# Kernel tuning notes

Measured on AMD Instinct MI355X. Metric: run time of the kernel, lower is better.

## Reference

```python
import jax, jax.numpy as jnp
import numpy as np
from jax import lax

# ---- static config (from BasePllay_2 / AdTopoLayer(out_features=50, T=25, m0=0.2, lims=[[224,0],[0,224]], K_max=2, p=0)) ----
H = W = 28
G = H * W
T = 25
K_MAX = 2
M0 = 0.2
OUT_FEATURES = 50
B = 32
TSEQ = jnp.linspace(0.0, 100.0, T)  # fixed landscape sample grid (covers DTM value range)

# static grid geometry from lims=[[224,0],[0,224]]
_xs = np.linspace(224.0, 0.0, H)
_ys = np.linspace(0.0, 224.0, W)
_pts = np.stack(np.meshgrid(_xs, _ys, indexing="ij"), -1).reshape(G, 2)
_d = np.sqrt(((_pts[:, None] - _pts[None]) ** 2).sum(-1))
_sidx = np.argsort(_d, axis=-1)
SDIST = jnp.asarray(np.take_along_axis(_d, _sidx, -1), jnp.float32)  # [G,G] sorted distances per grid point
SIDX = jnp.asarray(_sidx.astype(np.int32))                            # [G,G] static distance-sort order

# 4-connectivity neighbor table for the cubical (pixel) grid, -1 = invalid
_ii = np.arange(G).reshape(H, W)
_nb = np.full((H, W, 4), -1, np.int32)
_nb[1:, :, 0] = _ii[:-1, :]
_nb[:-1, :, 1] = _ii[1:, :]
_nb[:, 1:, 2] = _ii[:, :-1]
_nb[:, :-1, 3] = _ii[:, 1:]
NBR = jnp.asarray(_nb.reshape(G, 4))


def dtm(w):
    """Weighted distance-to-measure (r=2) on the fixed grid. w: [B,G] nonneg -> [B,G]."""
    sw = w[:, SIDX]                               # [B,G,G] weights in distance order
    cw = jnp.cumsum(sw, -1)
    d2 = SDIST ** 2
    cwd = jnp.cumsum(sw * d2[None], -1)
    bound = M0 * w.sum(-1)                        # [B]
    k = jnp.argmax(cw >= bound[:, None, None], -1)  # [B,G] first index reaching mass bound
    km1 = jnp.maximum(k - 1, 0)
    take = lambda a, i: jnp.take_along_axis(a, i[..., None], -1)[..., 0]
    has_prev = k > 0
    cw_p = jnp.where(has_prev, take(cw, km1), 0.0)
    cwd_p = jnp.where(has_prev, take(cwd, km1), 0.0)
    dk2 = d2[jnp.arange(G)[None, :], k]           # [B,G]
    val = (cwd_p + (bound[:, None] - cw_p) * dk2) / bound[:, None]
    return jnp.sqrt(jnp.maximum(val, 0.0))


def pd0(vals):
    """0-dim sublevel-set persistence of vals on the pixel grid (union-find, elder rule).
    Returns (births[G], deaths[G]); non-merging pixels yield zero-persistence pairs,
    essential components die at the max filtration value."""
    order = jnp.argsort(vals).astype(jnp.int32)
    rank = jnp.zeros(G, jnp.int32).at[order].set(jnp.arange(G, dtype=jnp.int32))

    def find(parent, i):
        return lax.while_loop(lambda j: parent[j] != j, lambda j: parent[j], i)

    def step(s, carry):
        parent, death = carry
        p = order[s]
        best = p
        for t in range(4):  # unrolled over the 4 grid neighbors (static)
            q = NBR[p, t]
            ok = (q >= 0) & (rank[jnp.maximum(q, 0)] < s)  # neighbor already inserted
            r = find(parent, jnp.where(ok, q, p))
            merge = ok & (r != best)
            r_old = rank[r] < rank[best]
            older = jnp.where(r_old, r, best)
            younger = jnp.where(r_old, best, r)
            widx = jnp.where(merge, younger, G)   # slot G is a dummy
            parent = parent.at[widx].set(older)
            death = death.at[widx].set(p)         # younger component dies at pixel p
            best = jnp.where(merge, older, best)
        return parent, death

    parent0 = jnp.arange(G + 1, dtype=jnp.int32)
    death0 = jnp.full(G + 1, -1, jnp.int32)
    _, death = lax.fori_loop(0, G, step, (parent0, death0))
    d = death[:G]
    deaths = jnp.where(d >= 0, vals[jnp.maximum(d, 0)], vals.max())
    return vals, deaths


def landscape(births, deaths):
    """K_MAX persistence landscapes sampled at TSEQ. [B,G] -> [B, K_MAX*T]."""
    tb = TSEQ[None, :, None] - births[:, None, :]   # [B,T,G]
    td = deaths[:, None, :] - TSEQ[None, :, None]
    tent = jnp.maximum(jnp.minimum(tb, td), 0.0)
    topk = lax.top_k(tent, K_MAX)[0]                # [B,T,K]
    return jnp.transpose(topk, (0, 2, 1)).reshape(births.shape[0], K_MAX * T)


def _forward(x, w_land, b_land, w_fc, b_fc):
    w = x.reshape(x.shape[0], -1)          # nn.Flatten: pixel intensities as measure weights
    v = dtm(w)                             # [B,G]
    births, deaths = jax.vmap(pd0)(v)
    feats = landscape(births, deaths)      # [B, 50]
    xt = feats @ w_land.T + b_land         # AdTopoLayer output [B, out_features]
    signal = jnp.abs(lax.stop_gradient(xt)).sum(0)   # torch: x.detach().abs().sum(0)
    out = jnp.maximum(xt, 0.0) @ w_fc.T + b_fc       # fc(relu(x))
    return out, signal

_forward_jit = jax.jit(_forward)


def setup_inputs() -> dict:
    key = jax.random.key(0)
    k = jax.random.split(key, 4)
    x = jax.random.uniform(k[0], (B, 1, H, W), jnp.float32)  # image-like nonneg weights
    w_land = jax.random.normal(k[1], (OUT_FEATURES, K_MAX * T), jnp.float32) * 0.1
    b_land = jnp.zeros((OUT_FEATURES,), jnp.float32)
    w_fc = jax.random.normal(k[2], (10, OUT_FEATURES), jnp.float32) * 0.1
    b_fc = jnp.zeros((10,), jnp.float32)
    return {"x": x, "w_land": w_land, "b_land": b_land, "w_fc": w_fc, "b_fc": b_fc}


def reference(x, w_land, b_land, w_fc, b_fc):
    return _forward_jit(x, w_land, b_land, w_fc, b_fc)
```

## Files before the change

kernel.cpp:

```cpp
#include <hip/hip_runtime.h>
#include <math.h>

#define H28 28
#define G784 784
#define BATCH 32
#define NOFF 3025
#define NOFFP 3072
#define NKEY 1459
#define TPTS 25
#define KMAX 2
#define NFEAT 50
#define OUTF 50
#define NCLS 10

#define NBX 16
#define BT 512
#define BT2 512

struct OffPair { unsigned ij; float d2; };
struct OffTab  { OffPair e[NOFFP]; };

constexpr double csqrt(double x) {
  double r = x * 0.5 + 1.0;
  for (int i = 0; i < 20; i++) r = 0.5 * (r + x / r);
  return r;
}

constexpr OffTab make_offtab() {
  OffTab t{};
  int start[NKEY] = {};
  for (int i = 0; i < NOFF; i++) {
    int di = i / 55 - 27, dj = i % 55 - 27;
    start[di * di + dj * dj]++;
  }
  int run = 0;
  for (int k = 0; k < NKEY; k++) { int h = start[k]; start[k] = run; run += h; }
  for (int i = 0; i < NOFF; i++) {
    int di = i / 55 - 27, dj = i % 55 - 27;
    int key = di * di + dj * dj;
    int pos = start[key]++;
    float sd = (key == 0) ? 0.0f : (float)(csqrt((double)key) * (224.0 / 27.0));
    t.e[pos].ij = ((unsigned)(di & 0xffff)) | (((unsigned)(dj & 0xffff)) << 16);
    t.e[pos].d2 = sd * sd;
  }
  for (int i = NOFF; i < NOFFP; i++) { t.e[i].ij = 0x00640064u; t.e[i].d2 = 0.f; }
  return t;
}

__device__ constexpr OffTab OFFTAB = make_offtab();

__device__ __forceinline__ float wave_iscan_f32(float x) {
  int t;
  t = __builtin_amdgcn_update_dpp(0, __float_as_int(x), 0x111, 0xf, 0xf, true);
  x += __int_as_float(t);
  t = __builtin_amdgcn_update_dpp(0, __float_as_int(x), 0x112, 0xf, 0xf, true);
  x += __int_as_float(t);
  t = __builtin_amdgcn_update_dpp(0, __float_as_int(x), 0x114, 0xf, 0xf, true);
  x += __int_as_float(t);
  t = __builtin_amdgcn_update_dpp(0, __float_as_int(x), 0x118, 0xf, 0xf, true);
  x += __int_as_float(t);
  t = __builtin_amdgcn_update_dpp(0, __float_as_int(x), 0x142, 0xa, 0xf, true);
  x += __int_as_float(t);
  t = __builtin_amdgcn_update_dpp(0, __float_as_int(x), 0x143, 0xc, 0xf, true);
  x += __int_as_float(t);
  return x;
}

__global__ __launch_bounds__(BT) void dtm_kernel(const float* __restrict__ x,
                                                 float* __restrict__ v,
                                                 int* __restrict__ done_ctr) {
  __shared__ float w_s[G784];
  __shared__ float red[BT];

  const int tid = threadIdx.x;
  const int b   = blockIdx.x;
  const int bx  = blockIdx.y;

  if (b == 0 && bx == 0 && tid == 0) *done_ctr = 0;

  float ps = 0.f;
  for (int i = tid; i < G784; i += BT) {
    float wv = x[b * G784 + i];
    w_s[i] = wv;
    ps += wv;
  }
  red[tid] = ps;
  __syncthreads();
  for (int off = BT / 2; off > 0; off >>= 1) {
    if (tid < off) red[tid] += red[tid + off];
    __syncthreads();
  }
  const float bound = 0.2f * red[0];

  const int wave = tid >> 6;
  const int lane = tid & 63;
  const int slot = bx * 8 + wave;

  for (int g = slot; g < G784; g += NBX * 8) {
    const int i1 = g / H28, j1 = g % H28;
    float cw = 0.f, cwd = 0.f;
    float cwp = 0.f, cwdp = 0.f, dk2 = 0.f;
    bool crossed = false;
    int o = lane;
    unsigned ij = OFFTAB.e[o].ij;
    float d2v   = OFFTAB.e[o].d2;
    for (int base = 0; base < NOFFP && !crossed; base += 64) {
      int onext = o + 64;
      if (onext >= NOFFP) onext = o;
      const unsigned ij_n = OFFTAB.e[onext].ij;
      const float    d2_n = OFFTAB.e[onext].d2;
      const int di = (short)(ij & 0xffffu);
      const int dj = (short)(ij >> 16);
      const int i2 = i1 + di, j2 = j1 + dj;
      const bool inb = ((unsigned)i2 < (unsigned)H28) & ((unsigned)j2 < (unsigned)H28);
      const float wv = inb ? w_s[i2 * H28 + j2] : 0.f;
      const float wd = wv * d2v;
      const float psw = wave_iscan_f32(wv);
      const float psd = wave_iscan_f32(wd);
      const unsigned long long mask = __ballot(cw + psw >= bound);
      if (mask) {
        const int f = __ffsll((unsigned long long)mask) - 1;
        const float psw_f = __shfl(psw, f);
        const float w_f   = __shfl(wv, f);
        const float psd_f = __shfl(psd, f);
        const float wd_f  = __shfl(wd, f);
        dk2  = __shfl(d2v, f);
        cwp  = cw + (psw_f - w_f);
        cwdp = cwd + (psd_f - wd_f);
        crossed = true;
      } else {
        cw  += __int_as_float(__builtin_amdgcn_readlane(__float_as_int(psw), 63));
        cwd += __int_as_float(__builtin_amdgcn_readlane(__float_as_int(psd), 63));
      }
      ij = ij_n; d2v = d2_n; o = onext;
    }
    const float val = (cwdp + (bound - cwp) * dk2) / bound;
    if (lane == 0) v[b * G784 + g] = sqrtf(fmaxf(val, 0.f));
  }
}

__device__ __forceinline__ unsigned long long pix_key(const float* val_s, int p) {
  return (((unsigned long long)__float_as_uint(val_s[p])) << 10) | (unsigned)p;
}

__global__ __launch_bounds__(BT2) void pd0_kernel(const float* __restrict__ v,
                                                  float* __restrict__ feats,
                                                  int* __restrict__ done_ctr,
                                                  const float* __restrict__ w_land,
                                                  const float* __restrict__ b_land,
                                                  const float* __restrict__ w_fc,
                                                  const float* __restrict__ b_fc,
                                                  float* __restrict__ out) {
  __shared__ float val_s[G784];
  __shared__ int   ptr_s[G784];
  __shared__ int   parent[G784];
  __shared__ float deathv[G784];
  __shared__ int   mlist[G784];
  __shared__ unsigned long long edges[2048];
  __shared__ float redf[BT2];
  __shared__ int   mcnt_sh, ecnt_sh, last_sh;
  __shared__ float vmax_sh;
  __shared__ float f_s[BATCH * NFEAT];
  __shared__ float xt_s[BATCH * OUTF];

  const int tid = threadIdx.x;
  const int b   = blockIdx.x;
  if (tid == 0) { mcnt_sh = 0; ecnt_sh = 0; }

  float pm = -1e30f;
  for (int i = tid; i < G784; i += BT2) {
    float xv = v[b * G784 + i];
    val_s[i] = xv;
    pm = fmaxf(pm, xv);
  }
  redf[tid] = pm;
  __syncthreads();
  for (int off = BT2 / 2; off > 0; off >>= 1) {
    if (tid < off) redf[tid] = fmaxf(redf[tid], redf[tid + off]);
    __syncthreads();
  }
  if (tid == 0) vmax_sh = redf[0];
  __syncthreads();
  const float vmax = vmax_sh;

  for (int p = tid; p < G784; p += BT2) {
    unsigned long long kp = pix_key(val_s, p);
    int i = p / H28, j = p % H28;
    int nbs[4];
    nbs[0] = (i > 0)       ? p - H28 : -1;
    nbs[1] = (i < H28 - 1) ? p + H28 : -1;
    nbs[2] = (j > 0)       ? p - 1   : -1;
    nbs[3] = (j < H28 - 1) ? p + 1   : -1;
    int best = p;
    unsigned long long bk = kp;
    for (int t = 0; t < 4; t++) {
      int q = nbs[t];
      if (q >= 0) {
        unsigned long long kq = pix_key(val_s, q);
        if (kq < bk) { bk = kq; best = q; }
      }
    }
    ptr_s[p]  = best;
    parent[p] = p;
    deathv[p] = vmax;
    if (best == p) {
      int mi = atomicAdd(&mcnt_sh, 1);
      mlist[mi] = p;
    }
  }
  __syncthreads();

  for (int r = 0; r < 10; r++) {
    for (int p = tid; p < G784; p += BT2) ptr_s[p] = ptr_s[ptr_s[p]];
    __syncthreads();
  }

  for (int p = tid; p < G784; p += BT2) {
    unsigned long long kp = pix_key(val_s, p);
    int i = p / H28, j = p % H28;
    int nbs[4];
    nbs[0] = (i > 0)       ? p - H28 : -1;
    nbs[1] = (i < H28 - 1) ? p + H28 : -1;
    nbs[2] = (j > 0)       ? p - 1   : -1;
    nbs[3] = (j < H28 - 1) ? p + 1   : -1;
    int bp = ptr_s[p];
    for (int t = 0; t < 4; t++) {
      int q = nbs[t];
      if (q >= 0) {
        unsigned long long kq = pix_key(val_s, q);
        int bq = ptr_s[q];
        if (kq < kp && bq != bp) {
          int e = atomicAdd(&ecnt_sh, 1);
          if (e < 2048)
            edges[e] = (((unsigned long long)__float_as_uint(val_s[p])) << 32) |
                       (((unsigned long long)(unsigned)p) << 22) |
                       (((unsigned long long)(unsigned)t) << 20) |
                       (((unsigned long long)(unsigned)bp) << 10) |
                       ((unsigned long long)(unsigned)bq);
        }
      }
    }
  }
  __syncthreads();
  const int ecnt = (ecnt_sh < 2048) ? ecnt_sh : 2048;
  const int mcnt = mcnt_sh;

  int n2 = 2;
  while (n2 < ecnt) n2 <<= 1;
  for (int i = ecnt + tid; i < n2; i += BT2) edges[i] = ~0ULL;
  __syncthreads();
  for (int kk = 2; kk <= n2; kk <<= 1) {
    for (int jj = kk >> 1; jj > 0; jj >>= 1) {
      for (int i = tid; i < n2; i += BT2) {
        int ixj = i ^ jj;
        if (ixj > i) {
          unsigned long long a = edges[i], c = edges[ixj];
          bool up = ((i & kk) == 0);
          if ((a > c) == up) { edges[i] = c; edges[ixj] = a; }
        }
      }
      __syncthreads();
    }
  }

  if (tid < 64) {
    const int target = mcnt - 1;
    int merged = 0;
    for (int base = 0; base < ecnt && merged < target; base += 64) {
      int i = base + tid;
      bool valid = (i < ecnt);
      unsigned long long e = valid ? edges[i] : 0ULL;
      int A = (int)((e >> 10) & 1023u);
      int B = (int)(e & 1023u);
      int rA = valid ? A : 0;
      int rB = valid ? B : 0;
      for (;;) { int pa = parent[rA]; bool mv = (pa != rA); rA = pa; if (!__any(mv)) break; }
      for (;;) { int pb = parent[rB]; bool mv = (pb != rB); rB = pb; if (!__any(mv)) break; }
      unsigned long long mask = __ballot(valid && (rA != rB));
      while (mask && merged < target) {
        int j = __ffsll(mask) - 1;
        mask &= mask - 1;
        unsigned long long ej = edges[base + j];
        int Aj = (int)((ej >> 10) & 1023u);
        int Bj = (int)(ej & 1023u);
        int ra = Aj; for (;;) { int pa = parent[ra]; if (pa == ra) break; ra = pa; }
        int rb = Bj; for (;;) { int pb = parent[rb]; if (pb == rb) break; rb = pb; }
        if (ra != rb) {
          unsigned long long ka = pix_key(val_s, ra);
          unsigned long long kb = pix_key(val_s, rb);
          int older   = (ka < kb) ? ra : rb;
          int younger = (ka < kb) ? rb : ra;
          parent[younger] = older;
          deathv[younger] = __uint_as_float((unsigned)(ej >> 32));
          merged++;
        }
      }
    }
  }
  __syncthreads();

  if (tid < TPTS) {
    float ti = (float)((double)tid * (100.0 / 24.0));
    float t1 = 0.f, t2 = 0.f;
    for (int ii = 0; ii < mcnt; ii++) {
      int m = mlist[ii];
      float tent = fminf(ti - val_s[m], deathv[m] - ti);
      tent = fmaxf(tent, 0.f);
      if (tent > t1)      { t2 = t1; t1 = tent; }
      else if (tent > t2) { t2 = tent; }
    }
    feats[b * NFEAT + tid]        = t1;
    feats[b * NFEAT + TPTS + tid] = t2;
  }

  __threadfence();
  __syncthreads();
  if (tid == 0) last_sh = (atomicAdd(done_ctr, 1) == BATCH - 1) ? 1 : 0;
  __syncthreads();
  if (!last_sh) return;
  __threadfence();

  for (int i = tid; i < BATCH * NFEAT; i += BT2) f_s[i] = feats[i];
  __syncthreads();
  for (int idx = tid; idx < BATCH * OUTF; idx += BT2) {
    int bb = idx / OUTF, ff = idx % OUTF;
    float acc = b_land[ff];
    const float* wr = w_land + ff * NFEAT;
    const float* fr = f_s + bb * NFEAT;
    for (int j = 0; j < NFEAT; j++) acc += fr[j] * wr[j];
    xt_s[idx] = acc;
  }
  __syncthreads();
  if (tid < OUTF) {
    float s = 0.f;
    for (int bb = 0; bb < BATCH; bb++) s += fabsf(xt_s[bb * OUTF + tid]);
    out[BATCH * NCLS + tid] = s;
  }
  for (int idx = tid; idx < BATCH * NCLS; idx += BT2) {
    int bb = idx / NCLS, cc = idx % NCLS;
    float acc = b_fc[cc];
    const float* wr = w_fc + cc * OUTF;
    const float* xr = xt_s + bb * OUTF;
    for (int ff = 0; ff < OUTF; ff++) acc += fmaxf(xr[ff], 0.f) * wr[ff];
    out[bb * NCLS + cc] = acc;
  }
}

extern "C" void kernel_launch(void* const* d_in, const int* in_sizes, int n_in,
                              void* d_out, int out_size, void* d_ws, size_t ws_size,
                              hipStream_t stream) {
  (void)in_sizes; (void)n_in; (void)out_size; (void)ws_size;
  const float* x      = (const float*)d_in[0];
  const float* w_land = (const float*)d_in[1];
  const float* b_land = (const float*)d_in[2];
  const float* w_fc   = (const float*)d_in[3];
  const float* b_fc   = (const float*)d_in[4];
  float* out   = (float*)d_out;
  float* v     = (float*)d_ws;
  float* feats = v + BATCH * G784;
  int*   done  = (int*)(feats + BATCH * NFEAT);

  dim3 g1(BATCH, NBX);
  dtm_kernel<<<g1, BT, 0, stream>>>(x, v, done);
  pd0_kernel<<<BATCH, BT2, 0, stream>>>(v, feats, done,
                                        w_land, b_land, w_fc, b_fc, out);
}
```

Before: 115.1 us.

## Deduplicate basin-pair edges via shared hash and merge with union-by-rank in one wave

Candidate merge edges between basins are deduplicated per basin pair using a shared-memory open-addressing hash that keeps only the minimum edge key per pair. The bitonic sort is done by a single wavefront, with no block-wide barriers, on the smaller edge set. Union-find now uses union-by-rank with path halving, tracks the oldest key per root, and merges in parallel within a wave using claim-based conflict resolution. The aim is to cut sort length, barriers and serial merge steps, at the cost of hash atomics, extra shared memory, and more delicate wave-level synchronisation correctness.

```diff
diff --git a/kernel.cpp b/kernel.cpp
--- a/kernel.cpp
+++ b/kernel.cpp
@@ -16,6 +16,8 @@
 #define NBX 16
 #define BT 512
 #define BT2 512
+#define HS 2048
+#define EMAX 1024
 
 struct OffPair { unsigned ij; float d2; };
 struct OffTab  { OffPair e[NOFFP]; };
@@ -154,9 +156,14 @@
   __shared__ float val_s[G784];
   __shared__ int   ptr_s[G784];
   __shared__ int   parent[G784];
+  __shared__ unsigned rank_s[G784];
+  __shared__ unsigned claims[G784];
   __shared__ float deathv[G784];
   __shared__ int   mlist[G784];
-  __shared__ unsigned long long edges[2048];
+  __shared__ unsigned long long oldkey[G784];
+  __shared__ unsigned htag[HS];
+  __shared__ unsigned long long hval[HS];
+  __shared__ unsigned long long edges[EMAX];
   __shared__ float redf[BT2];
   __shared__ int   mcnt_sh, ecnt_sh, last_sh;
   __shared__ float vmax_sh;
@@ -167,11 +174,15 @@
   const int b   = blockIdx.x;
   if (tid == 0) { mcnt_sh = 0; ecnt_sh = 0; }
 
+  for (int i = tid; i < HS; i += BT2) { htag[i] = 0u; hval[i] = ~0ULL; }
+
   float pm = -1e30f;
   for (int i = tid; i < G784; i += BT2) {
     float xv = v[b * G784 + i];
     val_s[i] = xv;
     pm = fmaxf(pm, xv);
+    rank_s[i] = 0u;
+    claims[i] = 0xFFFFFFFFu;
   }
   redf[tid] = pm;
   __syncthreads();
@@ -204,6 +215,7 @@
     parent[p] = p;
     deathv[p] = vmax;
     if (best == p) {
+      oldkey[p] = kp;
       int mi = atomicAdd(&mcnt_sh, 1);
       mlist[mi] = p;
     }
@@ -230,87 +242,127 @@
         unsigned long long kq = pix_key(val_s, q);
         int bq = ptr_s[q];
         if (kq < kp && bq != bp) {
-          int e = atomicAdd(&ecnt_sh, 1);
-          if (e < 2048)
-            edges[e] = (((unsigned long long)__float_as_uint(val_s[p])) << 32) |
-                       (((unsigned long long)(unsigned)p) << 22) |
-                       (((unsigned long long)(unsigned)t) << 20) |
-                       (((unsigned long long)(unsigned)bp) << 10) |
-                       ((unsigned long long)(unsigned)bq);
+          unsigned long long key =
+              (((unsigned long long)__float_as_uint(val_s[p])) << 32) |
+              (((unsigned long long)(unsigned)p) << 22) |
+              (((unsigned long long)(unsigned)t) << 20) |
+              (((unsigned long long)(unsigned)bp) << 10) |
+              ((unsigned long long)(unsigned)bq);
+          unsigned lo = (bp < bq) ? (unsigned)bp : (unsigned)bq;
+          unsigned hi = (bp < bq) ? (unsigned)bq : (unsigned)bp;
+          unsigned pairid = (lo << 10) | hi;
+          unsigned idx = (pairid * 2654435761u) >> 21;
+          for (;;) {
+            unsigned t0 = atomicCAS(&htag[idx], 0u, pairid + 1u);
+            if (t0 == 0u || t0 == pairid + 1u) { atomicMin(&hval[idx], key); break; }
+            idx = (idx + 1) & (HS - 1);
+          }
         }
       }
     }
   }
   __syncthreads();
-  const int ecnt = (ecnt_sh < 2048) ? ecnt_sh : 2048;
+
+  for (int i = tid; i < HS; i += BT2) {
+    if (htag[i]) {
+      int e = atomicAdd(&ecnt_sh, 1);
+      if (e < EMAX) edges[e] = hval[i];
+    }
+  }
+  __syncthreads();
+  const int ne   = (ecnt_sh < EMAX) ? ecnt_sh : EMAX;
   const int mcnt = mcnt_sh;
-
-  int n2 = 2;
-  while (n2 < ecnt) n2 <<= 1;
-  for (int i = ecnt + tid; i < n2; i += BT2) edges[i] = ~0ULL;
-  __syncthreads();
-  for (int kk = 2; kk <= n2; kk <<= 1) {
-    for (int jj = kk >> 1; jj > 0; jj >>= 1) {
-      for (int i = tid; i < n2; i += BT2) {
-        int ixj = i ^ jj;
-        if (ixj > i) {
-          unsigned long long a = edges[i], c = edges[ixj];
-          bool up = ((i & kk) == 0);
-          if ((a > c) == up) { edges[i] = c; edges[ixj] = a; }
+  const int wave = tid >> 6;
+  const int lane = tid & 63;
+
+  if (wave == 0) {
+    if (ne > 1) {
+      int n2 = 1;
+      while (n2 < ne) n2 <<= 1;
+      for (int i = ne + lane; i < n2; i += 64) edges[i] = ~0ULL;
+      __threadfence_block();
+      for (int kk = 2; kk <= n2; kk <<= 1) {
+        for (int jj = kk >> 1; jj > 0; jj >>= 1) {
+          for (int i = lane; i < n2; i += 64) {
+            int ixj = i ^ jj;
+            if (ixj > i) {
+              unsigned long long a = edges[i], c = edges[ixj];
+              bool up = ((i & kk) == 0);
+              if ((a > c) == up) { edges[i] = c; edges[ixj] = a; }
+            }
+          }
+          __threadfence_block();
         }
       }
-      __syncthreads();
-    }
-  }
-
-  if (tid < 64) {
+    }
+
+    int merged = 0;
     const int target = mcnt - 1;
-    int merged = 0;
-    for (int base = 0; base < ecnt && merged < target; base += 64) {
-      int i = base + tid;
-      bool valid = (i < ecnt);
-      unsigned long long e = valid ? edges[i] : 0ULL;
-      int A = (int)((e >> 10) & 1023u);
-      int B = (int)(e & 1023u);
-      int rA = valid ? A : 0;
-      int rB = valid ? B : 0;
-      for (;;) { int pa = parent[rA]; bool mv = (pa != rA); rA = pa; if (!__any(mv)) break; }
-      for (;;) { int pb = parent[rB]; bool mv = (pb != rB); rB = pb; if (!__any(mv)) break; }
-      unsigned long long mask = __ballot(valid && (rA != rB));
-      while (mask && merged < target) {
-        int j = __ffsll(mask) - 1;
-        mask &= mask - 1;
-        unsigned long long ej = edges[base + j];
-        int Aj = (int)((ej >> 10) & 1023u);
-        int Bj = (int)(ej & 1023u);
-        int ra = Aj; for (;;) { int pa = parent[ra]; if (pa == ra) break; ra = pa; }
-        int rb = Bj; for (;;) { int pb = parent[rb]; if (pb == rb) break; rb = pb; }
-        if (ra != rb) {
-          unsigned long long ka = pix_key(val_s, ra);
-          unsigned long long kb = pix_key(val_s, rb);
-          int older   = (ka < kb) ? ra : rb;
-          int younger = (ka < kb) ? rb : ra;
-          parent[younger] = older;
-          deathv[younger] = __uint_as_float((unsigned)(ej >> 32));
-          merged++;
+    for (int base = 0; base < ne && merged < target; base += 64) {
+      const int idx = base + lane;
+      bool unresolved = (idx < ne);
+      const unsigned long long e = unresolved ? edges[idx] : 0ULL;
+      const int A  = (int)((e >> 10) & 1023u);
+      const int Bq = (int)(e & 1023u);
+      const float ev = __uint_as_float((unsigned)(e >> 32));
+      for (;;) {
+        int rA = A, rB = Bq;
+        if (unresolved) {
+          int xx = A;
+          for (;;) { int p1 = parent[xx]; if (p1 == xx) break;
+                     int p2 = parent[p1]; parent[xx] = p2; xx = p2; }
+          rA = xx;
+          xx = Bq;
+          for (;;) { int p1 = parent[xx]; if (p1 == xx) break;
+                     int p2 = parent[p1]; parent[xx] = p2; xx = p2; }
+          rB = xx;
         }
-      }
-    }
-  }
-  __syncthreads();
-
-  if (tid < TPTS) {
-    float ti = (float)((double)tid * (100.0 / 24.0));
-    float t1 = 0.f, t2 = 0.f;
-    for (int ii = 0; ii < mcnt; ii++) {
-      int m = mlist[ii];
-      float tent = fminf(ti - val_s[m], deathv[m] - ti);
-      tent = fmaxf(tent, 0.f);
-      if (tent > t1)      { t2 = t1; t1 = tent; }
-      else if (tent > t2) { t2 = tent; }
-    }
-    feats[b * NFEAT + tid]        = t1;
-    feats[b * NFEAT + TPTS + tid] = t2;
+        bool crossing = unresolved && (rA != rB);
+        if (unresolved && !crossing) unresolved = false;
+        if (__ballot(crossing) == 0ULL) break;
+        if (crossing) {
+          atomicMin(&claims[rA], (unsigned)lane);
+          atomicMin(&claims[rB], (unsigned)lane);
+        }
+        __threadfence_block();
+        bool win = crossing && claims[rA] == (unsigned)lane
+                            && claims[rB] == (unsigned)lane;
+        __threadfence_block();
+        if (crossing) { claims[rA] = 0xFFFFFFFFu; claims[rB] = 0xFFFFFFFFu; }
+        if (win) {
+          unsigned long long ka = oldkey[rA], kb = oldkey[rB];
+          unsigned ra_ = rank_s[rA], rb_ = rank_s[rB];
+          int big   = (ra_ > rb_) ? rA : ((rb_ > ra_) ? rB : ((rA < rB) ? rA : rB));
+          int small = (big == rA) ? rB : rA;
+          parent[small] = big;
+          if (ra_ == rb_) rank_s[big] = ra_ + 1u;
+          unsigned long long okmin = (ka < kb) ? ka : kb;
+          unsigned long long okmax = (ka < kb) ? kb : ka;
+          oldkey[big] = okmin;
+          int dying = (int)(okmax & 1023u);
+          deathv[dying] = ev;
+          unresolved = false;
+        }
+        __threadfence_block();
+        merged += (int)__popcll(__ballot(win));
+        if (merged >= target) break;
+      }
+    }
+    __threadfence_block();
+
+    if (lane < TPTS) {
+      float ti = (float)((double)lane * (100.0 / 24.0));
+      float t1 = 0.f, t2 = 0.f;
+      for (int ii = 0; ii < mcnt; ii++) {
+        int m = mlist[ii];
+        float tent = fminf(ti - val_s[m], deathv[m] - ti);
+        tent = fmaxf(tent, 0.f);
+        if (tent > t1)      { t2 = t1; t1 = tent; }
+        else if (tent > t2) { t2 = tent; }
+      }
+      feats[b * NFEAT + lane]        = t1;
+      feats[b * NFEAT + TPTS + lane] = t2;
+    }
   }
 
   __threadfence();
```

Result: faster. 100.5 us (-12.7%).
